# Kernel tuning notes

Hardware: AMD Instinct MI355X
Metric: run time of the kernel (lower is better)

The kernel has to match this reference:

```python
import jax, jax.numpy as jnp
import numpy as np

D_MODEL = 192
D_STATE = 16
D_CONV = 4
EXPAND = 2
D_INNER = EXPAND * D_MODEL
DT_RANK = (D_MODEL + 15) // 16  # ceil(d_model/16) = 12


def setup_inputs() -> dict:
    key = jax.random.key(0)
    ks = jax.random.split(key, 12)
    B, C, H, W = 16, D_MODEL, 64, 64
    s = lambda n: 0.02
    return {
        "x": jax.random.normal(ks[0], (B, C, H, W), jnp.float32),
        "ln_g": jnp.ones((C,), jnp.float32),
        "ln_b": jnp.zeros((C,), jnp.float32),
        "W_in": jax.random.normal(ks[1], (D_MODEL, 2 * D_INNER), jnp.float32) * s(0),
        "conv_w": jax.random.normal(ks[2], (D_INNER, D_CONV), jnp.float32) * 0.1,
        "conv_b": jnp.zeros((D_INNER,), jnp.float32),
        "W_x": jax.random.normal(ks[3], (D_INNER, DT_RANK + 2 * D_STATE), jnp.float32) * s(0),
        "W_dt": jax.random.normal(ks[4], (DT_RANK, D_INNER), jnp.float32) * 0.1,
        "b_dt": jax.random.uniform(ks[5], (D_INNER,), jnp.float32, -4.0, -1.0),
        "A_log": jnp.log(jnp.broadcast_to(jnp.arange(1, D_STATE + 1, dtype=jnp.float32), (D_INNER, D_STATE))),
        "Dp": jnp.ones((D_INNER,), jnp.float32),
        "W_out": jax.random.normal(ks[6], (D_INNER, D_MODEL), jnp.float32) * s(0),
    }


def _layernorm2d(x, g, b, eps=1e-5):
    # x: (B, C, H, W); normalize over channel dim
    mu = jnp.mean(x, axis=1, keepdims=True)
    var = jnp.var(x, axis=1, keepdims=True)
    xn = (x - mu) * jax.lax.rsqrt(var + eps)
    return xn * g[None, :, None, None] + b[None, :, None, None]


def _mamba(x, W_in, conv_w, conv_b, W_x, W_dt, b_dt, A_log, Dp, W_out):
    # x: (B, L, d_model)
    B, L, _ = x.shape
    xz = x @ W_in                       # (B, L, 2*d_inner)
    xi, z = jnp.split(xz, 2, axis=-1)   # each (B, L, d_inner)

    # causal depthwise conv over L
    xc = jnp.transpose(xi, (0, 2, 1))   # (B, d_inner, L)
    k = conv_w[:, None, :]              # (d_inner, 1, d_conv)
    xc = jax.lax.conv_general_dilated(
        xc, k, window_strides=(1,), padding=[(D_CONV - 1, 0)],
        dimension_numbers=("NCH", "OIH", "NCH"), feature_group_count=D_INNER)
    xc = xc + conv_b[None, :, None]
    u = jax.nn.silu(jnp.transpose(xc, (0, 2, 1)))  # (B, L, d_inner)

    xdbc = u @ W_x                      # (B, L, dt_rank + 2*d_state)
    dt_r, Bm, Cm = jnp.split(xdbc, [DT_RANK, DT_RANK + D_STATE], axis=-1)
    dt = jax.nn.softplus(dt_r @ W_dt + b_dt)  # (B, L, d_inner)
    A = -jnp.exp(A_log)                 # (d_inner, d_state)

    def step(h, inp):
        u_t, dt_t, B_t, C_t = inp       # (B,di), (B,di), (B,ds), (B,ds)
        dA = jnp.exp(dt_t[..., None] * A)              # (B, di, ds)
        dBu = (dt_t * u_t)[..., None] * B_t[:, None, :]  # (B, di, ds)
        h = h * dA + dBu
        y = jnp.einsum("bds,bs->bd", h, C_t)
        return h, y

    h0 = jnp.zeros((B, D_INNER, D_STATE), x.dtype)
    seq = (jnp.moveaxis(u, 1, 0), jnp.moveaxis(dt, 1, 0),
           jnp.moveaxis(Bm, 1, 0), jnp.moveaxis(Cm, 1, 0))
    _, ys = jax.lax.scan(step, h0, seq)
    y = jnp.moveaxis(ys, 0, 1) + u * Dp  # (B, L, d_inner)
    y = y * jax.nn.silu(z)
    return y @ W_out                    # (B, L, d_model)


def reference(x, ln_g, ln_b, W_in, conv_w, conv_b, W_x, W_dt, b_dt, A_log, Dp, W_out):
    b, c, h, w = x.shape
    residual = x
    xn = _layernorm2d(x, ln_g, ln_b)
    seq = jnp.transpose(xn.reshape(b, c, h * w), (0, 2, 1))  # (B, L, C)
    out = _mamba(seq, W_in, conv_w, conv_b, W_x, W_dt, b_dt, A_log, Dp, W_out)
    out = jnp.transpose(out, (0, 2, 1)).reshape(b, c, h, w)
    return out + residual
```

## Files before the change

### kernel.cpp

```cpp
#include <hip/hip_runtime.h>

typedef unsigned short u16;
typedef unsigned int u32;
typedef __attribute__((ext_vector_type(8))) short short8;
typedef __attribute__((ext_vector_type(4))) float f32x4;
typedef __attribute__((ext_vector_type(2))) float f32x2;

#define DEV __device__ __forceinline__

DEV float b2f(u16 u) { union { u32 i; float f; } v; v.i = ((u32)u) << 16; return v.f; }
DEV u16 f2b(float f) {
  union { float f; u32 i; } v; v.f = f;
  u32 r = v.i + 0x7FFFu + ((v.i >> 16) & 1u);
  return (u16)(r >> 16);
}
DEV bool sniff_f32(const void* ln_g) { return ((const u32*)ln_g)[0] == 0x3F800000u; }
DEV float rdv(const void* p, size_t i, bool f32) {
  return f32 ? ((const float*)p)[i] : b2f(((const u16*)p)[i]);
}

__global__ __launch_bounds__(256) void k0_prep(
    const void* __restrict__ W_in, const void* __restrict__ W_out,
    const void* __restrict__ W_x, const void* __restrict__ W_dt,
    const void* __restrict__ b_dt, const void* __restrict__ conv_w,
    const void* __restrict__ conv_b, const void* __restrict__ A_log,
    const void* __restrict__ Dp, const void* __restrict__ ln_g,
    const void* __restrict__ ln_b,
    u16* __restrict__ WinT, u16* __restrict__ WoutT, u16* __restrict__ WbigT,
    float* __restrict__ BdtF, float* __restrict__ convW, float* __restrict__ convB,
    float* __restrict__ AlnF, float* __restrict__ DpF,
    float* __restrict__ lnG, float* __restrict__ lnB) {
  const bool f32 = sniff_f32(ln_g);
  int i = blockIdx.x * 256 + threadIdx.x;
  if (i < 147456) { int n = i / 192, k = i - n * 192; WinT[i] = f2b(rdv(W_in, (size_t)k * 768 + n, f32)); return; }
  i -= 147456;
  if (i < 73728) { int c = i / 384, d = i - c * 384; WoutT[i] = f2b(rdv(W_out, (size_t)d * 192 + c, f32)); return; }
  i -= 73728;
  if (i < 196608) {
    int n = i / 384, k = i - n * 384;
    float v;
    if (n < 384) {
      v = 0.f;
      for (int r = 0; r < 12; ++r)
        v = fmaf(rdv(W_x, (size_t)k * 44 + r, f32), rdv(W_dt, (size_t)r * 384 + n, f32), v);
    } else if (n < 400) {
      v = rdv(W_x, (size_t)k * 44 + 12 + (n - 384), f32);
    } else if (n < 416) {
      v = rdv(W_x, (size_t)k * 44 + 28 + (n - 400), f32);
    } else {
      v = 0.f;
    }
    WbigT[i] = f2b(v);
    return;
  }
  i -= 196608;
  if (i < 384) { BdtF[i] = rdv(b_dt, i, f32); return; }
  i -= 384;
  if (i < 1536) { convW[i] = rdv(conv_w, i, f32); return; }
  i -= 1536;
  if (i < 384) { convB[i] = rdv(conv_b, i, f32); return; }
  i -= 384;
  if (i < 6144) { AlnF[i] = -__expf(rdv(A_log, i, f32)); return; }
  i -= 6144;
  if (i < 384) { DpF[i] = rdv(Dp, i, f32); return; }
  i -= 384;
  if (i < 192) { lnG[i] = rdv(ln_g, i, f32); return; }
  i -= 192;
  if (i < 192) { lnB[i] = rdv(ln_b, i, f32); return; }
}

__global__ __launch_bounds__(192) void k1_ln(
    const void* __restrict__ xg, const void* __restrict__ lng_raw,
    const float* __restrict__ lnG, const float* __restrict__ lnB,
    u16* __restrict__ xn) {
  const bool f32 = sniff_f32(lng_raw);
  const int b = blockIdx.y, l0 = blockIdx.x * 64, t = threadIdx.x;
  __shared__ float xs[192][65];
  __shared__ float rs[3][64], rq[3][64], smu[64], srstd[64];

  for (int i = t; i < 192 * 64; i += 192) {
    int c = i >> 6, l = i & 63;
    xs[c][l] = rdv(xg, ((size_t)(b * 192 + c)) * 4096 + l0 + l, f32);
  }
  __syncthreads();
  const int part = t >> 6, l = t & 63;
  float s = 0.f, q2 = 0.f;
  for (int cc = 0; cc < 64; ++cc) {
    float v = xs[part * 64 + cc][l];
    s += v; q2 = fmaf(v, v, q2);
  }
  rs[part][l] = s; rq[part][l] = q2;
  __syncthreads();
  if (t < 64) {
    float S = rs[0][t] + rs[1][t] + rs[2][t];
    float Q = rq[0][t] + rq[1][t] + rq[2][t];
    float mu = S * (1.0f / 192.0f);
    float var = Q * (1.0f / 192.0f) - mu * mu;
    smu[t] = mu; srstd[t] = rsqrtf(var + 1e-5f);
  }
  __syncthreads();
  const float gv = lnG[t], bv = lnB[t];
  for (int ll = 0; ll < 64; ++ll) {
    float v = (xs[t][ll] - smu[ll]) * srstd[ll];
    xn[((size_t)(b * 4096 + l0 + ll)) * 192 + t] = f2b(fmaf(v, gv, bv));
  }
}

__global__ __launch_bounds__(256) void k2_gemm1(
    const u16* __restrict__ WinT, const u16* __restrict__ xn,
    u16* __restrict__ xz) {
  const int ch0 = blockIdx.x * 128, l0 = blockIdx.y * 128, b = blockIdx.z;
  const int tid = threadIdx.x;
  const int wave = tid >> 6, lane = tid & 63;
  const int wr = wave >> 1, wc = wave & 1;
  const int q = lane >> 4, lm = lane & 15;

  __shared__ __align__(16) u16 As[128][72];
  __shared__ __align__(16) u16 Bs[128][72];

  f32x4 acc[4][4];
#pragma unroll
  for (int i = 0; i < 4; ++i)
#pragma unroll
    for (int j = 0; j < 4; ++j) acc[i][j] = (f32x4){0.f, 0.f, 0.f, 0.f};

  const int r4 = tid >> 3, c8 = (tid & 7) * 8;

  for (int kb = 0; kb < 3; ++kb) {
    const int c0 = kb * 64;
    __syncthreads();
#pragma unroll
    for (int p = 0; p < 4; ++p) {
      int r = p * 32 + r4;
      *(uint4*)&As[r][c8] = *(const uint4*)(WinT + (size_t)(ch0 + r) * 192 + c0 + c8);
      *(uint4*)&Bs[r][c8] = *(const uint4*)(xn + ((size_t)b * 4096 + l0 + r) * 192 + c0 + c8);
    }
    __syncthreads();
#pragma unroll
    for (int ks = 0; ks < 2; ++ks) {
      short8 a[4], bfr[4];
#pragma unroll
      for (int mt = 0; mt < 4; ++mt)
        a[mt] = *(const short8*)&As[wr * 64 + mt * 16 + lm][ks * 32 + q * 8];
#pragma unroll
      for (int nt = 0; nt < 4; ++nt)
        bfr[nt] = *(const short8*)&Bs[wc * 64 + nt * 16 + lm][ks * 32 + q * 8];
#pragma unroll
      for (int mt = 0; mt < 4; ++mt)
#pragma unroll
        for (int nt = 0; nt < 4; ++nt)
          acc[mt][nt] = __builtin_amdgcn_mfma_f32_16x16x32_bf16(a[mt], bfr[nt], acc[mt][nt], 0, 0, 0);
    }
  }
#pragma unroll
  for (int mt = 0; mt < 4; ++mt)
#pragma unroll
    for (int nt = 0; nt < 4; ++nt) {
      int n = l0 + wc * 64 + nt * 16 + lm;
#pragma unroll
      for (int reg = 0; reg < 4; ++reg) {
        int m = ch0 + wr * 64 + mt * 16 + q * 4 + reg;
        xz[((size_t)b * 768 + m) * 4096 + n] = f2b(acc[mt][nt][reg]);
      }
    }
}

__global__ __launch_bounds__(256) void k3_conv(
    u16* __restrict__ xz, const float* __restrict__ convW,
    const float* __restrict__ convB) {
  const int d = blockIdx.x, b = blockIdx.y, t = threadIdx.x;
  u16* row = xz + ((size_t)b * 768 + d) * 4096;
  __shared__ __align__(16) u16 srow[4096];
#pragma unroll
  for (int p = 0; p < 2; ++p)
    *(uint4*)&srow[p * 2048 + t * 8] = *(const uint4*)(row + p * 2048 + t * 8);
  __syncthreads();
  const float w0 = convW[d * 4 + 0], w1 = convW[d * 4 + 1];
  const float w2 = convW[d * 4 + 2], w3 = convW[d * 4 + 3];
  const float cb = convB[d];
  const int l = t * 16;
  u16 o[16];
#pragma unroll
  for (int i = 0; i < 16; ++i) {
    int li = l + i;
    float x0 = (li >= 3) ? b2f(srow[li - 3]) : 0.f;
    float x1 = (li >= 2) ? b2f(srow[li - 2]) : 0.f;
    float x2 = (li >= 1) ? b2f(srow[li - 1]) : 0.f;
    float x3 = b2f(srow[li]);
    float s = w0 * x0 + w1 * x1 + w2 * x2 + w3 * x3 + cb;
    float sig = 1.0f / (1.0f + __expf(-s));
    o[i] = f2b(s * sig);
  }
#pragma unroll
  for (int i = 0; i < 4; ++i) {
    ushort4 st; st.x = o[i * 4 + 0]; st.y = o[i * 4 + 1];
    st.z = o[i * 4 + 2]; st.w = o[i * 4 + 3];
    *(ushort4*)(row + l + i * 4) = st;
  }
}

__global__ __launch_bounds__(256) void k4_mfma(
    const u16* __restrict__ WbigT, const u16* __restrict__ xz,
    const float* __restrict__ BdtF,
    u16* __restrict__ dtb, float* __restrict__ Btl, float* __restrict__ Ctl) {
  const int ch0 = blockIdx.x * 128, l0 = blockIdx.y * 128, b = blockIdx.z;
  const int tid = threadIdx.x;
  const int wave = tid >> 6, lane = tid & 63;
  const int wr = wave >> 1, wc = wave & 1;
  const int q = lane >> 4, lm = lane & 15;

  __shared__ __align__(16) u16 As[128][72];
  __shared__ __align__(16) u16 Bs[128][72];

  f32x4 acc[4][4];
#pragma unroll
  for (int i = 0; i < 4; ++i)
#pragma unroll
    for (int j = 0; j < 4; ++j) acc[i][j] = (f32x4){0.f, 0.f, 0.f, 0.f};

  const int r4 = tid >> 3, c8 = (tid & 7) * 8;
  const int rb = tid >> 5, l4b = (tid & 31) * 4;

  for (int kb = 0; kb < 6; ++kb) {
    const int d0 = kb * 64;
    __syncthreads();
#pragma unroll
    for (int p = 0; p < 4; ++p) {
      int r = p * 32 + r4;
      *(uint4*)&As[r][c8] = *(const uint4*)(WbigT + (size_t)(ch0 + r) * 384 + d0 + c8);
    }
#pragma unroll
    for (int p = 0; p < 8; ++p) {
      int dd = p * 8 + rb;
      ushort4 vv = *(const ushort4*)(xz + ((size_t)b * 768 + d0 + dd) * 4096 + l0 + l4b);
      const int g = dd >> 3, d7 = dd & 7;
      const u16 vals[4] = {vv.x, vv.y, vv.z, vv.w};
#pragma unroll
      for (int i = 0; i < 4; ++i) {
        int l = l4b + i;
        int sc = (((g ^ ((l >> 2) & 7)) << 3) | d7);
        Bs[l][sc] = vals[i];
      }
    }
    __syncthreads();
#pragma unroll
    for (int ks = 0; ks < 2; ++ks) {
      short8 a[4], bfr[4];
#pragma unroll
      for (int mt = 0; mt < 4; ++mt)
        a[mt] = *(const short8*)&As[wr * 64 + mt * 16 + lm][ks * 32 + q * 8];
#pragma unroll
      for (int nt = 0; nt < 4; ++nt) {
        int row = wc * 64 + nt * 16 + lm;
        int g2 = (ks * 4 + q) ^ ((row >> 2) & 7);
        bfr[nt] = *(const short8*)&Bs[row][g2 * 8];
      }
#pragma unroll
      for (int mt = 0; mt < 4; ++mt)
#pragma unroll
        for (int nt = 0; nt < 4; ++nt)
          acc[mt][nt] = __builtin_amdgcn_mfma_f32_16x16x32_bf16(a[mt], bfr[nt], acc[mt][nt], 0, 0, 0);
    }
  }
#pragma unroll
  for (int mt = 0; mt < 4; ++mt) {
    const int tbase = ch0 + wr * 64 + mt * 16;
#pragma unroll
    for (int nt = 0; nt < 4; ++nt) {
      const int l = l0 + wc * 64 + nt * 16 + lm;
      if (tbase < 384) {
#pragma unroll
        for (int reg = 0; reg < 4; ++reg) {
          int m = tbase + q * 4 + reg;
          float v = acc[mt][nt][reg] + BdtF[m];
          float sp = __logf(1.0f + __expf(v));
          dtb[((size_t)b * 384 + m) * 4096 + l] = f2b(sp);
        }
      } else if (tbase == 384) {
        float4 v; v.x = acc[mt][nt][0]; v.y = acc[mt][nt][1];
        v.z = acc[mt][nt][2]; v.w = acc[mt][nt][3];
        *(float4*)(Btl + (((size_t)b * 4096 + l) << 4) + q * 4) = v;
      } else if (tbase == 400) {
        float4 v; v.x = acc[mt][nt][0]; v.y = acc[mt][nt][1];
        v.z = acc[mt][nt][2]; v.w = acc[mt][nt][3];
        *(float4*)(Ctl + (((size_t)b * 4096 + l) << 4) + q * 4) = v;
      }
    }
  }
}

#define NCH 128
#define TCH 32

DEV void build_e8p(float dt, const float* ap, int sbase, bool powok, f32x2* e2) {
  if (powok) {
    float q1 = __expf(-dt);
    float q2 = q1 * q1, q3 = q2 * q1, q4 = q2 * q2;
    float q5 = q4 * q1, q6 = q4 * q2, q7 = q4 * q3, q8 = q4 * q4;
    f32x2 m2; m2.x = sbase ? q8 : 1.0f; m2.y = m2.x;
    f32x2 a0; a0.x = q1; a0.y = q2;
    f32x2 a1; a1.x = q3; a1.y = q4;
    f32x2 a2; a2.x = q5; a2.y = q6;
    f32x2 a3; a3.x = q7; a3.y = q8;
    e2[0] = a0 * m2; e2[1] = a1 * m2; e2[2] = a2 * m2; e2[3] = a3 * m2;
  } else {
#pragma unroll
    for (int k = 0; k < 4; ++k) {
      f32x2 v;
      v.x = __expf(dt * ap[sbase + 2 * k]);
      v.y = __expf(dt * ap[sbase + 2 * k + 1]);
      e2[k] = v;
    }
  }
}

__global__ __launch_bounds__(256) void k5a_part(
    const u16* __restrict__ dtg, const u16* __restrict__ xz,
    const float* __restrict__ Btl, const float* __restrict__ AlnF,
    u16* __restrict__ Sbuf, float* __restrict__ sumdt) {
  const int cx = blockIdx.x, b = blockIdx.z;
  const int t = threadIdx.x;
  const int wave = t >> 6, lane = t & 63;
  const int dg0 = blockIdx.y * 128;
  const int sh = lane >> 5, dl = lane & 31;
  const int sbase = sh * 8;
  const int lc = cx * TCH;
  __shared__ __align__(16) u16 sdt[128][40], su[128][40];
  __shared__ __align__(16) float sB[TCH][16];
#pragma unroll
  for (int i = t; i < 512; i += 256) {
    int r = i >> 2, c8 = (i & 3) * 8;
    *(uint4*)&sdt[r][c8] = *(const uint4*)(dtg + ((size_t)b * 384 + dg0 + r) * 4096 + lc + c8);
    *(uint4*)&su[r][c8] = *(const uint4*)(xz + ((size_t)b * 768 + dg0 + r) * 4096 + lc + c8);
  }
  if (t < 128) {
    int r = t >> 2, c4 = (t & 3) * 4;
    *(float4*)&sB[r][c4] = *(const float4*)(Btl + (((size_t)b * 4096 + lc + r) << 4) + c4);
  }
  __syncthreads();

  const int dr = wave * 32 + dl;
  const int d = dg0 + dr;
  const float* ap = AlnF + d * 16;
  bool powok = true;
#pragma unroll
  for (int k = 0; k < 8; ++k)
    powok = powok && (fabsf(ap[sbase + k] + (float)(sbase + k + 1)) < 1e-3f * (float)(sbase + k + 1));

  f32x2 S2[4];
#pragma unroll
  for (int k = 0; k < 4; ++k) S2[k] = (f32x2){0.f, 0.f};
  float sdsum = 0.f;

#pragma unroll 1
  for (int l8 = 0; l8 < TCH / 8; ++l8) {
    short8 d8 = *(const short8*)&sdt[dr][l8 * 8];
    short8 u8 = *(const short8*)&su[dr][l8 * 8];
#pragma unroll
    for (int j = 0; j < 8; ++j) {
      float dt = b2f((u16)d8[j]);
      float uu = b2f((u16)u8[j]);
      float dtu = dt * uu;
      sdsum += dt;
      f32x2 e2[4];
      build_e8p(dt, ap, sbase, powok, e2);
      const float* Bp = &sB[l8 * 8 + j][sbase];
      float4 Bv0 = *(const float4*)(Bp);
      float4 Bv1 = *(const float4*)(Bp + 4);
      f32x2 dtu2; dtu2.x = dtu; dtu2.y = dtu;
      f32x2 b0; b0.x = Bv0.x; b0.y = Bv0.y;
      f32x2 b1; b1.x = Bv0.z; b1.y = Bv0.w;
      f32x2 b2; b2.x = Bv1.x; b2.y = Bv1.y;
      f32x2 b3; b3.x = Bv1.z; b3.y = Bv1.w;
      S2[0] = S2[0] * e2[0] + dtu2 * b0;
      S2[1] = S2[1] * e2[1] + dtu2 * b1;
      S2[2] = S2[2] * e2[2] + dtu2 * b2;
      S2[3] = S2[3] * e2[3] + dtu2 * b3;
    }
  }
  const size_t base = (((size_t)b * NCH + cx) * 384 + d) * 16 + sbase;
  u32 w[4];
#pragma unroll
  for (int k = 0; k < 4; ++k)
    w[k] = (u32)f2b(S2[k].x) | ((u32)f2b(S2[k].y) << 16);
  uint4 st0; st0.x = w[0]; st0.y = w[1]; st0.z = w[2]; st0.w = w[3];
  *(uint4*)(Sbuf + base) = st0;
  if (sh == 0)
    sumdt[((size_t)b * NCH + cx) * 384 + d] = sdsum;
}

__global__ __launch_bounds__(256) void k5b_comb(
    u16* __restrict__ Sbuf, const float* __restrict__ sumdt,
    const float* __restrict__ AlnF) {
  const int idx = blockIdx.x * 256 + threadIdx.x;
  const int s = idx & 15;
  const int bd = idx >> 4;
  const int b = bd / 384;
  const int d = bd - b * 384;
  const float a = AlnF[d * 16 + s];
  const size_t cstride = 384 * 16;
  const size_t base0 = ((size_t)b * NCH) * cstride + (size_t)d * 16 + s;
  const float* sdp = sumdt + (size_t)b * NCH * 384 + d;
  float h = 0.f;
  float Sv_next = b2f(Sbuf[base0]);
  float sd_next = sdp[0];
  for (int c = 0; c < NCH; ++c) {
    float Sv = Sv_next, sd = sd_next;
    if (c + 1 < NCH) {
      Sv_next = b2f(Sbuf[base0 + (size_t)(c + 1) * cstride]);
      sd_next = sdp[(size_t)(c + 1) * 384];
    }
    Sbuf[base0 + (size_t)c * cstride] = f2b(h);
    h = fmaf(h, __expf(a * sd), Sv);
  }
}

__global__ __launch_bounds__(256) void k5c_scan(
    const u16* __restrict__ dtg, u16* __restrict__ xz,
    const float* __restrict__ Btl, const float* __restrict__ Ctl,
    const u16* __restrict__ Sbuf, const float* __restrict__ AlnF,
    const float* __restrict__ DpF) {
  const int cx = blockIdx.x, b = blockIdx.z;
  const int t = threadIdx.x;
  const int wave = t >> 6, lane = t & 63;
  const int dg0 = blockIdx.y * 128;
  const int sh = lane >> 5, dl = lane & 31;
  const int sbase = sh * 8;
  const int lc = cx * TCH;
  __shared__ __align__(16) u16 sdt[128][40], su[128][40], sz[128][40];
  __shared__ __align__(16) float sB[TCH][16], sC[TCH][16];
#pragma unroll
  for (int i = t; i < 512; i += 256) {
    int r = i >> 2, c8 = (i & 3) * 8;
    *(uint4*)&sdt[r][c8] = *(const uint4*)(dtg + ((size_t)b * 384 + dg0 + r) * 4096 + lc + c8);
    *(uint4*)&su[r][c8] = *(const uint4*)(xz + ((size_t)b * 768 + dg0 + r) * 4096 + lc + c8);
    *(uint4*)&sz[r][c8] = *(const uint4*)(xz + ((size_t)b * 768 + 384 + dg0 + r) * 4096 + lc + c8);
  }
  if (t < 128) {
    int r = t >> 2, c4 = (t & 3) * 4;
    *(float4*)&sB[r][c4] = *(const float4*)(Btl + (((size_t)b * 4096 + lc + r) << 4) + c4);
    *(float4*)&sC[r][c4] = *(const float4*)(Ctl + (((size_t)b * 4096 + lc + r) << 4) + c4);
  }
  __syncthreads();

  const int dr = wave * 32 + dl;
  const int d = dg0 + dr;
  const float* ap = AlnF + d * 16;
  bool powok = true;
#pragma unroll
  for (int k = 0; k < 8; ++k)
    powok = powok && (fabsf(ap[sbase + k] + (float)(sbase + k + 1)) < 1e-3f * (float)(sbase + k + 1));
  const float Dpl = DpF[d];

  f32x2 h2[4];
  {
    const size_t base = (((size_t)b * NCH + cx) * 384 + d) * 16 + sbase;
    uint4 s0 = *(const uint4*)(Sbuf + base);
    const u32 w[4] = {s0.x, s0.y, s0.z, s0.w};
#pragma unroll
    for (int k = 0; k < 4; ++k) {
      f32x2 v; v.x = b2f((u16)(w[k] & 0xFFFF)); v.y = b2f((u16)(w[k] >> 16));
      h2[k] = v;
    }
  }

  u16* zrow = xz + ((size_t)b * 768 + 384 + d) * 4096;

#pragma unroll 1
  for (int l8 = 0; l8 < TCH / 8; ++l8) {
    short8 d8 = *(const short8*)&sdt[dr][l8 * 8];
    short8 u8 = *(const short8*)&su[dr][l8 * 8];
    short8 z8 = *(const short8*)&sz[dr][l8 * 8];
    float yh[8];
#pragma unroll
    for (int j = 0; j < 8; ++j) {
      float dt = b2f((u16)d8[j]);
      float uu = b2f((u16)u8[j]);
      float dtu = dt * uu;
      f32x2 e2[4];
      build_e8p(dt, ap, sbase, powok, e2);
      const float* Bp = &sB[l8 * 8 + j][sbase];
      const float* Cp = &sC[l8 * 8 + j][sbase];
      float4 Bv0 = *(const float4*)(Bp);
      float4 Bv1 = *(const float4*)(Bp + 4);
      float4 Cv0 = *(const float4*)(Cp);
      float4 Cv1 = *(const float4*)(Cp + 4);
      f32x2 dtu2; dtu2.x = dtu; dtu2.y = dtu;
      f32x2 b0; b0.x = Bv0.x; b0.y = Bv0.y;
      f32x2 b1; b1.x = Bv0.z; b1.y = Bv0.w;
      f32x2 b2; b2.x = Bv1.x; b2.y = Bv1.y;
      f32x2 b3; b3.x = Bv1.z; b3.y = Bv1.w;
      f32x2 c0; c0.x = Cv0.x; c0.y = Cv0.y;
      f32x2 c1; c1.x = Cv0.z; c1.y = Cv0.w;
      f32x2 c2; c2.x = Cv1.x; c2.y = Cv1.y;
      f32x2 c3; c3.x = Cv1.z; c3.y = Cv1.w;
      h2[0] = h2[0] * e2[0] + dtu2 * b0;
      h2[1] = h2[1] * e2[1] + dtu2 * b1;
      h2[2] = h2[2] * e2[2] + dtu2 * b2;
      h2[3] = h2[3] * e2[3] + dtu2 * b3;
      f32x2 y2 = h2[0] * c0;
      y2 = h2[1] * c1 + y2;
      y2 = h2[2] * c2 + y2;
      y2 = h2[3] * c3 + y2;
      yh[j] = y2.x + y2.y;
    }
    u32 ya[4];
#pragma unroll
    for (int j = 0; j < 8; ++j) {
      float yfull = yh[j] + __shfl_xor(yh[j], 32, 64);
      float uu2 = b2f((u16)u8[j]);
      float zz2 = b2f((u16)z8[j]);
      float yf = fmaf(uu2, Dpl, yfull);
      float sig = 1.0f / (1.0f + __expf(-zz2));
      yf *= zz2 * sig;
      u16 yb = f2b(yf);
      if (j & 1) ya[j >> 1] |= ((u32)yb << 16);
      else ya[j >> 1] = (u32)yb;
    }
    if (sh == 0) {
      uint4 st; st.x = ya[0]; st.y = ya[1]; st.z = ya[2]; st.w = ya[3];
      *(uint4*)(zrow + lc + l8 * 8) = st;
    }
  }
}

__global__ __launch_bounds__(256) void k6_gemm2(
    const u16* __restrict__ WoutT, const u16* __restrict__ xz,
    const void* __restrict__ xg, const void* __restrict__ lng_raw,
    void* __restrict__ outg) {
  const bool f32 = sniff_f32(lng_raw);
  const int l0 = blockIdx.x * 128, b = blockIdx.y;
  const int tid = threadIdx.x;
  const int wave = tid >> 6, lane = tid & 63;
  const int wm = wave >> 1, wn = wave & 1;
  const int q = lane >> 4, lm = lane & 15;

  __shared__ __align__(16) u16 As[192][72];
  __shared__ __align__(16) u16 Bs[128][72];

  f32x4 acc[6][4];
#pragma unroll
  for (int i = 0; i < 6; ++i)
#pragma unroll
    for (int j = 0; j < 4; ++j) acc[i][j] = (f32x4){0.f, 0.f, 0.f, 0.f};

  const int ra = tid >> 3, c8 = (tid & 7) * 8;
  const int rb = tid >> 5, l4b = (tid & 31) * 4;

  for (int kb = 0; kb < 6; ++kb) {
    const int d0 = kb * 64;
    __syncthreads();
#pragma unroll
    for (int p = 0; p < 6; ++p) {
      int r = p * 32 + ra;
      *(uint4*)&As[r][c8] = *(const uint4*)(WoutT + (size_t)r * 384 + d0 + c8);
    }
#pragma unroll
    for (int p = 0; p < 8; ++p) {
      int dd = p * 8 + rb;
      ushort4 vv = *(const ushort4*)(xz + ((size_t)b * 768 + 384 + d0 + dd) * 4096 + l0 + l4b);
      const int g = dd >> 3, d7 = dd & 7;
      const u16 vals[4] = {vv.x, vv.y, vv.z, vv.w};
#pragma unroll
      for (int i = 0; i < 4; ++i) {
        int l = l4b + i;
        int sc = (((g ^ ((l >> 2) & 7)) << 3) | d7);
        Bs[l][sc] = vals[i];
      }
    }
    __syncthreads();
#pragma unroll
    for (int ks = 0; ks < 2; ++ks) {
      short8 a[6], bfr[4];
#pragma unroll
      for (int mt = 0; mt < 6; ++mt)
        a[mt] = *(const short8*)&As[wm * 96 + mt * 16 + lm][ks * 32 + q * 8];
#pragma unroll
      for (int nt = 0; nt < 4; ++nt) {
        int row = wn * 64 + nt * 16 + lm;
        int g2 = (ks * 4 + q) ^ ((row >> 2) & 7);
        bfr[nt] = *(const short8*)&Bs[row][g2 * 8];
      }
#pragma unroll
      for (int mt = 0; mt < 6; ++mt)
#pragma unroll
        for (int nt = 0; nt < 4; ++nt)
          acc[mt][nt] = __builtin_amdgcn_mfma_f32_16x16x32_bf16(a[mt], bfr[nt], acc[mt][nt], 0, 0, 0);
    }
  }
  if (f32) {
    float* op = (float*)outg;
    const float* xp = (const float*)xg;
#pragma unroll
    for (int mt = 0; mt < 6; ++mt)
#pragma unroll
      for (int nt = 0; nt < 4; ++nt) {
        int l = l0 + wn * 64 + nt * 16 + lm;
#pragma unroll
        for (int reg = 0; reg < 4; ++reg) {
          int m = wm * 96 + mt * 16 + q * 4 + reg;
          size_t idx = ((size_t)b * 192 + m) * 4096 + l;
          op[idx] = acc[mt][nt][reg] + xp[idx];
        }
      }
  } else {
    u16* op = (u16*)outg;
    const u16* xp = (const u16*)xg;
#pragma unroll
    for (int mt = 0; mt < 6; ++mt)
#pragma unroll
      for (int nt = 0; nt < 4; ++nt) {
        int l = l0 + wn * 64 + nt * 16 + lm;
#pragma unroll
        for (int reg = 0; reg < 4; ++reg) {
          int m = wm * 96 + mt * 16 + q * 4 + reg;
          size_t idx = ((size_t)b * 192 + m) * 4096 + l;
          op[idx] = f2b(acc[mt][nt][reg] + b2f(xp[idx]));
        }
      }
  }
}

extern "C" void kernel_launch(void* const* d_in, const int* in_sizes, int n_in,
                              void* d_out, int out_size, void* d_ws, size_t ws_size,
                              hipStream_t stream) {
  (void)in_sizes; (void)n_in; (void)out_size; (void)ws_size;
  const void* x      = d_in[0];
  const void* ln_g   = d_in[1];
  const void* ln_b   = d_in[2];
  const void* W_in   = d_in[3];
  const void* conv_w = d_in[4];
  const void* conv_b = d_in[5];
  const void* W_x    = d_in[6];
  const void* W_dt   = d_in[7];
  const void* b_dt   = d_in[8];
  const void* A_log  = d_in[9];
  const void* Dp     = d_in[10];
  const void* W_out  = d_in[11];

  char* ws = (char*)d_ws;
  u16*   xz    = (u16*)(ws + 0);
  u16*   xn    = (u16*)(ws + 100663296);
  u16*   dtb   = (u16*)(ws + 100663296);
  float* Btl   = (float*)(ws + 150994944);
  float* Ctl   = (float*)(ws + 155189248);
  u16*   Sbuf  = (u16*)(ws + 159383552);
  float* sumdt = (float*)(ws + 184549376);
  u16*   WinT  = (u16*)(ws + 187695104);
  u16*   WoutT = (u16*)(ws + 187990016);
  u16*   WbigT = (u16*)(ws + 188137472);
  float* BdtF  = (float*)(ws + 188530688);
  float* convW = (float*)(ws + 188532224);
  float* convB = (float*)(ws + 188538368);
  float* AlnF  = (float*)(ws + 188539904);
  float* DpF   = (float*)(ws + 188564480);
  float* lnG   = (float*)(ws + 188566016);
  float* lnB   = (float*)(ws + 188566784);

  k0_prep<<<dim3(1668), dim3(256), 0, stream>>>(
      W_in, W_out, W_x, W_dt, b_dt, conv_w, conv_b, A_log, Dp, ln_g, ln_b,
      WinT, WoutT, WbigT, BdtF, convW, convB, AlnF, DpF, lnG, lnB);
  k1_ln<<<dim3(64, 16), dim3(192), 0, stream>>>(x, ln_g, lnG, lnB, xn);
  k2_gemm1<<<dim3(6, 32, 16), dim3(256), 0, stream>>>(WinT, xn, xz);
  k3_conv<<<dim3(384, 16), dim3(256), 0, stream>>>(xz, convW, convB);
  k4_mfma<<<dim3(4, 32, 16), dim3(256), 0, stream>>>(WbigT, xz, BdtF, dtb, Btl, Ctl);
  k5a_part<<<dim3(NCH, 3, 16), dim3(256), 0, stream>>>(dtb, xz, Btl, AlnF, Sbuf, sumdt);
  k5b_comb<<<dim3(384), dim3(256), 0, stream>>>(Sbuf, sumdt, AlnF);
  k5c_scan<<<dim3(NCH, 3, 16), dim3(256), 0, stream>>>(dtb, xz, Btl, Ctl, Sbuf, AlnF, DpF);
  k6_gemm2<<<dim3(32, 16), dim3(256), 0, stream>>>(WoutT, xz, x, ln_g, (void*)d_out);
}
```

Before: 565.1 us.

## Give each scan thread all 16 states for one channel, dropping cross-lane shuffle

The chunked selective-scan kernels (partial and final) now assign one thread per channel holding all 16 state elements, instead of two half-waves each holding 8 states. This removes the shuffle-xor reduction of y and the duplicated dt/u/z decode and gating work, and halves the block size to 128 threads. The exp powers are built through a shared q1/q2/q4/q8 chain, and the shared-memory row pitch is reduced to 36 with 8-byte accesses. The cost is more registers per thread and half as many threads per block, which may reduce latency hiding.

After: 662.0 us. +17.1%, slower.

```diff
diff --git a/kernel.cpp b/kernel.cpp
--- a/kernel.cpp
+++ b/kernel.cpp
@@ -14,6 +14,8 @@
   u32 r = v.i + 0x7FFFu + ((v.i >> 16) & 1u);
   return (u16)(r >> 16);
 }
+DEV float lo2f(u32 w) { union { u32 i; float f; } v; v.i = w << 16; return v.f; }
+DEV float hi2f(u32 w) { union { u32 i; float f; } v; v.i = w & 0xFFFF0000u; return v.f; }
 DEV bool sniff_f32(const void* ln_g) { return ((const u32*)ln_g)[0] == 0x3F800000u; }
 DEV float rdv(const void* p, size_t i, bool f32) {
   return f32 ? ((const float*)p)[i] : b2f(((const u16*)p)[i]);
@@ -292,101 +294,98 @@
 #define NCH 128
 #define TCH 32
 
-DEV void build_e8p(float dt, const float* ap, int sbase, bool powok, f32x2* e2) {
-  if (powok) {
-    float q1 = __expf(-dt);
-    float q2 = q1 * q1, q3 = q2 * q1, q4 = q2 * q2;
-    float q5 = q4 * q1, q6 = q4 * q2, q7 = q4 * q3, q8 = q4 * q4;
-    f32x2 m2; m2.x = sbase ? q8 : 1.0f; m2.y = m2.x;
-    f32x2 a0; a0.x = q1; a0.y = q2;
-    f32x2 a1; a1.x = q3; a1.y = q4;
-    f32x2 a2; a2.x = q5; a2.y = q6;
-    f32x2 a3; a3.x = q7; a3.y = q8;
-    e2[0] = a0 * m2; e2[1] = a1 * m2; e2[2] = a2 * m2; e2[3] = a3 * m2;
-  } else {
-#pragma unroll
-    for (int k = 0; k < 4; ++k) {
-      f32x2 v;
-      v.x = __expf(dt * ap[sbase + 2 * k]);
-      v.y = __expf(dt * ap[sbase + 2 * k + 1]);
-      e2[k] = v;
-    }
-  }
-}
-
-__global__ __launch_bounds__(256) void k5a_part(
+__global__ __launch_bounds__(128) void k5a_part(
     const u16* __restrict__ dtg, const u16* __restrict__ xz,
     const float* __restrict__ Btl, const float* __restrict__ AlnF,
     u16* __restrict__ Sbuf, float* __restrict__ sumdt) {
   const int cx = blockIdx.x, b = blockIdx.z;
   const int t = threadIdx.x;
-  const int wave = t >> 6, lane = t & 63;
   const int dg0 = blockIdx.y * 128;
-  const int sh = lane >> 5, dl = lane & 31;
-  const int sbase = sh * 8;
   const int lc = cx * TCH;
-  __shared__ __align__(16) u16 sdt[128][40], su[128][40];
+  __shared__ __align__(16) u16 sdt[128][36], su[128][36];
   __shared__ __align__(16) float sB[TCH][16];
 #pragma unroll
-  for (int i = t; i < 512; i += 256) {
+  for (int i = t; i < 512; i += 128) {
     int r = i >> 2, c8 = (i & 3) * 8;
-    *(uint4*)&sdt[r][c8] = *(const uint4*)(dtg + ((size_t)b * 384 + dg0 + r) * 4096 + lc + c8);
-    *(uint4*)&su[r][c8] = *(const uint4*)(xz + ((size_t)b * 768 + dg0 + r) * 4096 + lc + c8);
-  }
-  if (t < 128) {
+    uint4 vd = *(const uint4*)(dtg + ((size_t)b * 384 + dg0 + r) * 4096 + lc + c8);
+    uint4 vu = *(const uint4*)(xz + ((size_t)b * 768 + dg0 + r) * 4096 + lc + c8);
+    *(uint2*)&sdt[r][c8] = make_uint2(vd.x, vd.y);
+    *(uint2*)&sdt[r][c8 + 4] = make_uint2(vd.z, vd.w);
+    *(uint2*)&su[r][c8] = make_uint2(vu.x, vu.y);
+    *(uint2*)&su[r][c8 + 4] = make_uint2(vu.z, vu.w);
+  }
+  {
     int r = t >> 2, c4 = (t & 3) * 4;
     *(float4*)&sB[r][c4] = *(const float4*)(Btl + (((size_t)b * 4096 + lc + r) << 4) + c4);
   }
   __syncthreads();
 
-  const int dr = wave * 32 + dl;
-  const int d = dg0 + dr;
+  const int d = dg0 + t;
   const float* ap = AlnF + d * 16;
   bool powok = true;
 #pragma unroll
-  for (int k = 0; k < 8; ++k)
-    powok = powok && (fabsf(ap[sbase + k] + (float)(sbase + k + 1)) < 1e-3f * (float)(sbase + k + 1));
-
-  f32x2 S2[4];
-#pragma unroll
-  for (int k = 0; k < 4; ++k) S2[k] = (f32x2){0.f, 0.f};
+  for (int k = 0; k < 16; ++k)
+    powok = powok && (fabsf(ap[k] + (float)(k + 1)) < 1e-3f * (float)(k + 1));
+
+  f32x2 S2[8];
+#pragma unroll
+  for (int k = 0; k < 8; ++k) S2[k] = (f32x2){0.f, 0.f};
   float sdsum = 0.f;
 
 #pragma unroll 1
   for (int l8 = 0; l8 < TCH / 8; ++l8) {
-    short8 d8 = *(const short8*)&sdt[dr][l8 * 8];
-    short8 u8 = *(const short8*)&su[dr][l8 * 8];
+    uint2 dA = *(const uint2*)&sdt[t][l8 * 8];
+    uint2 dB = *(const uint2*)&sdt[t][l8 * 8 + 4];
+    uint2 uA = *(const uint2*)&su[t][l8 * 8];
+    uint2 uB = *(const uint2*)&su[t][l8 * 8 + 4];
+    const u32 dw[4] = {dA.x, dA.y, dB.x, dB.y};
+    const u32 uw[4] = {uA.x, uA.y, uB.x, uB.y};
 #pragma unroll
     for (int j = 0; j < 8; ++j) {
-      float dt = b2f((u16)d8[j]);
-      float uu = b2f((u16)u8[j]);
+      float dt = (j & 1) ? hi2f(dw[j >> 1]) : lo2f(dw[j >> 1]);
+      float uu = (j & 1) ? hi2f(uw[j >> 1]) : lo2f(uw[j >> 1]);
       float dtu = dt * uu;
       sdsum += dt;
-      f32x2 e2[4];
-      build_e8p(dt, ap, sbase, powok, e2);
-      const float* Bp = &sB[l8 * 8 + j][sbase];
-      float4 Bv0 = *(const float4*)(Bp);
-      float4 Bv1 = *(const float4*)(Bp + 4);
+      f32x2 e2[8];
+      if (powok) {
+        float q1 = __expf(-dt);
+        float q2 = q1 * q1, q4 = q2 * q2, q8 = q4 * q4;
+        f32x2 E1; E1.x = q1; E1.y = q2;
+        f32x2 Q2; Q2.x = q2; Q2.y = q2;
+        f32x2 Q4; Q4.x = q4; Q4.y = q4;
+        f32x2 Q8; Q8.x = q8; Q8.y = q8;
+        e2[0] = E1;       e2[1] = E1 * Q2;
+        e2[2] = E1 * Q4;  e2[3] = e2[1] * Q4;
+        e2[4] = E1 * Q8;  e2[5] = e2[1] * Q8;
+        e2[6] = e2[2] * Q8; e2[7] = e2[3] * Q8;
+      } else {
+#pragma unroll
+        for (int k = 0; k < 8; ++k) {
+          f32x2 v;
+          v.x = __expf(dt * ap[2 * k]);
+          v.y = __expf(dt * ap[2 * k + 1]);
+          e2[k] = v;
+        }
+      }
+      const float* Bp = &sB[l8 * 8 + j][0];
       f32x2 dtu2; dtu2.x = dtu; dtu2.y = dtu;
-      f32x2 b0; b0.x = Bv0.x; b0.y = Bv0.y;
-      f32x2 b1; b1.x = Bv0.z; b1.y = Bv0.w;
-      f32x2 b2; b2.x = Bv1.x; b2.y = Bv1.y;
-      f32x2 b3; b3.x = Bv1.z; b3.y = Bv1.w;
-      S2[0] = S2[0] * e2[0] + dtu2 * b0;
-      S2[1] = S2[1] * e2[1] + dtu2 * b1;
-      S2[2] = S2[2] * e2[2] + dtu2 * b2;
-      S2[3] = S2[3] * e2[3] + dtu2 * b3;
-    }
-  }
-  const size_t base = (((size_t)b * NCH + cx) * 384 + d) * 16 + sbase;
-  u32 w[4];
-#pragma unroll
-  for (int k = 0; k < 4; ++k)
+#pragma unroll
+      for (int k = 0; k < 8; ++k) {
+        f32x2 bk; bk.x = Bp[2 * k]; bk.y = Bp[2 * k + 1];
+        S2[k] = S2[k] * e2[k] + dtu2 * bk;
+      }
+    }
+  }
+  const size_t base = (((size_t)b * NCH + cx) * 384 + d) * 16;
+  u32 w[8];
+#pragma unroll
+  for (int k = 0; k < 8; ++k)
     w[k] = (u32)f2b(S2[k].x) | ((u32)f2b(S2[k].y) << 16);
   uint4 st0; st0.x = w[0]; st0.y = w[1]; st0.z = w[2]; st0.w = w[3];
+  uint4 st1; st1.x = w[4]; st1.y = w[5]; st1.z = w[6]; st1.w = w[7];
   *(uint4*)(Sbuf + base) = st0;
-  if (sh == 0)
-    sumdt[((size_t)b * NCH + cx) * 384 + d] = sdsum;
+  *(uint4*)(Sbuf + base + 8) = st1;
+  sumdt[((size_t)b * NCH + cx) * 384 + d] = sdsum;
 }
 
 __global__ __launch_bounds__(256) void k5b_comb(
@@ -415,50 +414,53 @@
   }
 }
 
-__global__ __launch_bounds__(256) void k5c_scan(
+__global__ __launch_bounds__(128) void k5c_scan(
     const u16* __restrict__ dtg, u16* __restrict__ xz,
     const float* __restrict__ Btl, const float* __restrict__ Ctl,
     const u16* __restrict__ Sbuf, const float* __restrict__ AlnF,
     const float* __restrict__ DpF) {
   const int cx = blockIdx.x, b = blockIdx.z;
   const int t = threadIdx.x;
-  const int wave = t >> 6, lane = t & 63;
   const int dg0 = blockIdx.y * 128;
-  const int sh = lane >> 5, dl = lane & 31;
-  const int sbase = sh * 8;
   const int lc = cx * TCH;
-  __shared__ __align__(16) u16 sdt[128][40], su[128][40], sz[128][40];
+  __shared__ __align__(16) u16 sdt[128][36], su[128][36], sz[128][36];
   __shared__ __align__(16) float sB[TCH][16], sC[TCH][16];
 #pragma unroll
-  for (int i = t; i < 512; i += 256) {
+  for (int i = t; i < 512; i += 128) {
     int r = i >> 2, c8 = (i & 3) * 8;
-    *(uint4*)&sdt[r][c8] = *(const uint4*)(dtg + ((size_t)b * 384 + dg0 + r) * 4096 + lc + c8);
-    *(uint4*)&su[r][c8] = *(const uint4*)(xz + ((size_t)b * 768 + dg0 + r) * 4096 + lc + c8);
-    *(uint4*)&sz[r][c8] = *(const uint4*)(xz + ((size_t)b * 768 + 384 + dg0 + r) * 4096 + lc + c8);
-  }
-  if (t < 128) {
+    uint4 vd = *(const uint4*)(dtg + ((size_t)b * 384 + dg0 + r) * 4096 + lc + c8);
+    uint4 vu = *(const uint4*)(xz + ((size_t)b * 768 + dg0 + r) * 4096 + lc + c8);
+    uint4 vz = *(const uint4*)(xz + ((size_t)b * 768 + 384 + dg0 + r) * 4096 + lc + c8);
+    *(uint2*)&sdt[r][c8] = make_uint2(vd.x, vd.y);
+    *(uint2*)&sdt[r][c8 + 4] = make_uint2(vd.z, vd.w);
+    *(uint2*)&su[r][c8] = make_uint2(vu.x, vu.y);
+    *(uint2*)&su[r][c8 + 4] = make_uint2(vu.z, vu.w);
+    *(uint2*)&sz[r][c8] = make_uint2(vz.x, vz.y);
+    *(uint2*)&sz[r][c8 + 4] = make_uint2(vz.z, vz.w);
+  }
+  {
     int r = t >> 2, c4 = (t & 3) * 4;
     *(float4*)&sB[r][c4] = *(const float4*)(Btl + (((size_t)b * 4096 + lc + r) << 4) + c4);
     *(float4*)&sC[r][c4] = *(const float4*)(Ctl + (((size_t)b * 4096 + lc + r) << 4) + c4);
   }
   __syncthreads();
 
-  const int dr = wave * 32 + dl;
-  const int d = dg0 + dr;
+  const int d = dg0 + t;
   const float* ap = AlnF + d * 16;
   bool powok = true;
 #pragma unroll
-  for (int k = 0; k < 8; ++k)
-    powok = powok && (fabsf(ap[sbase + k] + (float)(sbase + k + 1)) < 1e-3f * (float)(sbase + k + 1));
+  for (int k = 0; k < 16; ++k)
+    powok = powok && (fabsf(ap[k] + (float)(k + 1)) < 1e-3f * (float)(k + 1));
   const float Dpl = DpF[d];
 
-  f32x2 h2[4];
+  f32x2 h2[8];
   {
-    const size_t base = (((size_t)b * NCH + cx) * 384 + d) * 16 + sbase;
+    const size_t base = (((size_t)b * NCH + cx) * 384 + d) * 16;
     uint4 s0 = *(const uint4*)(Sbuf + base);
-    const u32 w[4] = {s0.x, s0.y, s0.z, s0.w};
-#pragma unroll
-    for (int k = 0; k < 4; ++k) {
+    uint4 s1 = *(const uint4*)(Sbuf + base + 8);
+    const u32 w[8] = {s0.x, s0.y, s0.z, s0.w, s1.x, s1.y, s1.z, s1.w};
+#pragma unroll
+    for (int k = 0; k < 8; ++k) {
       f32x2 v; v.x = b2f((u16)(w[k] & 0xFFFF)); v.y = b2f((u16)(w[k] >> 16));
       h2[k] = v;
     }
@@ -468,59 +470,64 @@
 
 #pragma unroll 1
   for (int l8 = 0; l8 < TCH / 8; ++l8) {
-    short8 d8 = *(const short8*)&sdt[dr][l8 * 8];
-    short8 u8 = *(const short8*)&su[dr][l8 * 8];
-    short8 z8 = *(const short8*)&sz[dr][l8 * 8];
-    float yh[8];
+    uint2 dA = *(const uint2*)&sdt[t][l8 * 8];
+    uint2 dB = *(const uint2*)&sdt[t][l8 * 8 + 4];
+    uint2 uA = *(const uint2*)&su[t][l8 * 8];
+    uint2 uB = *(const uint2*)&su[t][l8 * 8 + 4];
+    uint2 zA = *(const uint2*)&sz[t][l8 * 8];
+    uint2 zB = *(const uint2*)&sz[t][l8 * 8 + 4];
+    const u32 dw[4] = {dA.x, dA.y, dB.x, dB.y};
+    const u32 uw[4] = {uA.x, uA.y, uB.x, uB.y};
+    const u32 zw[4] = {zA.x, zA.y, zB.x, zB.y};
+    u32 ya[4];
 #pragma unroll
     for (int j = 0; j < 8; ++j) {
-      float dt = b2f((u16)d8[j]);
-      float uu = b2f((u16)u8[j]);
+      float dt = (j & 1) ? hi2f(dw[j >> 1]) : lo2f(dw[j >> 1]);
+      float uu = (j & 1) ? hi2f(uw[j >> 1]) : lo2f(uw[j >> 1]);
+      float zz = (j & 1) ? hi2f(zw[j >> 1]) : lo2f(zw[j >> 1]);
       float dtu = dt * uu;
-      f32x2 e2[4];
-      build_e8p(dt, ap, sbase, powok, e2);
-      const float* Bp = &sB[l8 * 8 + j][sbase];
-      const float* Cp = &sC[l8 * 8 + j][sbase];
-      float4 Bv0 = *(const float4*)(Bp);
-      float4 Bv1 = *(const float4*)(Bp + 4);
-      float4 Cv0 = *(const float4*)(Cp);
-      float4 Cv1 = *(const float4*)(Cp + 4);
+      f32x2 e2[8];
+      if (powok) {
+        float q1 = __expf(-dt);
+        float q2 = q1 * q1, q4 = q2 * q2, q8 = q4 * q4;
+        f32x2 E1; E1.x = q1; E1.y = q2;
+        f32x2 Q2; Q2.x = q2; Q2.y = q2;
+        f32x2 Q4; Q4.x = q4; Q4.y = q4;
+        f32x2 Q8; Q8.x = q8; Q8.y = q8;
+        e2[0] = E1;       e2[1] = E1 * Q2;
+        e2[2] = E1 * Q4;  e2[3] = e2[1] * Q4;
+        e2[4] = E1 * Q8;  e2[5] = e2[1] * Q8;
+        e2[6] = e2[2] * Q8; e2[7] = e2[3] * Q8;
+      } else {
+#pragma unroll
+        for (int k = 0; k < 8; ++k) {
+          f32x2 v;
+          v.x = __expf(dt * ap[2 * k]);
+          v.y = __expf(dt * ap[2 * k + 1]);
+          e2[k] = v;
+        }
+      }
+      const float* Bp = &sB[l8 * 8 + j][0];
+      const float* Cp = &sC[l8 * 8 + j][0];
       f32x2 dtu2; dtu2.x = dtu; dtu2.y = dtu;
-      f32x2 b0; b0.x = Bv0.x; b0.y = Bv0.y;
-      f32x2 b1; b1.x = Bv0.z; b1.y = Bv0.w;
-      f32x2 b2; b2.x = Bv1.x; b2.y = Bv1.y;
-      f32x2 b3; b3.x = Bv1.z; b3.y = Bv1.w;
-      f32x2 c0; c0.x = Cv0.x; c0.y = Cv0.y;
-      f32x2 c1; c1.x = Cv0.z; c1.y = Cv0.w;
-      f32x2 c2; c2.x = Cv1.x; c2.y = Cv1.y;
-      f32x2 c3; c3.x = Cv1.z; c3.y = Cv1.w;
-      h2[0] = h2[0] * e2[0] + dtu2 * b0;
-      h2[1] = h2[1] * e2[1] + dtu2 * b1;
-      h2[2] = h2[2] * e2[2] + dtu2 * b2;
-      h2[3] = h2[3] * e2[3] + dtu2 * b3;
-      f32x2 y2 = h2[0] * c0;
-      y2 = h2[1] * c1 + y2;
-      y2 = h2[2] * c2 + y2;
-      y2 = h2[3] * c3 + y2;
-      yh[j] = y2.x + y2.y;
-    }
-    u32 ya[4];
-#pragma unroll
-    for (int j = 0; j < 8; ++j) {
-      float yfull = yh[j] + __shfl_xor(yh[j], 32, 64);
-      float uu2 = b2f((u16)u8[j]);
-      float zz2 = b2f((u16)z8[j]);
-      float yf = fmaf(uu2, Dpl, yfull);
-      float sig = 1.0f / (1.0f + __expf(-zz2));
-      yf *= zz2 * sig;
+      f32x2 y2; y2.x = 0.f; y2.y = 0.f;
+#pragma unroll
+      for (int k = 0; k < 8; ++k) {
+        f32x2 bk; bk.x = Bp[2 * k]; bk.y = Bp[2 * k + 1];
+        f32x2 ck; ck.x = Cp[2 * k]; ck.y = Cp[2 * k + 1];
+        h2[k] = h2[k] * e2[k] + dtu2 * bk;
+        y2 = y2 + h2[k] * ck;
+      }
+      float yfull = y2.x + y2.y;
+      float yf = fmaf(uu, Dpl, yfull);
+      float sig = 1.0f / (1.0f + __expf(-zz));
+      yf *= zz * sig;
       u16 yb = f2b(yf);
       if (j & 1) ya[j >> 1] |= ((u32)yb << 16);
       else ya[j >> 1] = (u32)yb;
     }
-    if (sh == 0) {
-      uint4 st; st.x = ya[0]; st.y = ya[1]; st.z = ya[2]; st.w = ya[3];
-      *(uint4*)(zrow + lc + l8 * 8) = st;
-    }
+    uint4 st; st.x = ya[0]; st.y = ya[1]; st.z = ya[2]; st.w = ya[3];
+    *(uint4*)(zrow + lc + l8 * 8) = st;
   }
 }
 
@@ -664,8 +671,8 @@
   k2_gemm1<<<dim3(6, 32, 16), dim3(256), 0, stream>>>(WinT, xn, xz);
   k3_conv<<<dim3(384, 16), dim3(256), 0, stream>>>(xz, convW, convB);
   k4_mfma<<<dim3(4, 32, 16), dim3(256), 0, stream>>>(WbigT, xz, BdtF, dtb, Btl, Ctl);
-  k5a_part<<<dim3(NCH, 3, 16), dim3(256), 0, stream>>>(dtb, xz, Btl, AlnF, Sbuf, sumdt);
+  k5a_part<<<dim3(NCH, 3, 16), dim3(128), 0, stream>>>(dtb, xz, Btl, AlnF, Sbuf, sumdt);
   k5b_comb<<<dim3(384), dim3(256), 0, stream>>>(Sbuf, sumdt, AlnF);
-  k5c_scan<<<dim3(NCH, 3, 16), dim3(256), 0, stream>>>(dtb, xz, Btl, Ctl, Sbuf, AlnF, DpF);
+  k5c_scan<<<dim3(NCH, 3, 16), dim3(128), 0, stream>>>(dtb, xz, Btl, Ctl, Sbuf, AlnF, DpF);
   k6_gemm2<<<dim3(32, 16), dim3(256), 0, stream>>>(WoutT, xz, x, ln_g, (void*)d_out);
 }
```
